# Performance work log

Measured on AMD Instinct MI355X. Metric: run time of the kernel, lower is better.

Reference implementation:

```python
import jax, jax.numpy as jnp
import numpy as np

THRESHOLD = 0.05   # area-ratio cutoff for 'small target'
SMOOTH = 1e-5      # dice smoothing
FG_FRAC = 0.02     # fraction of foreground pixels in synthetic target (< THRESHOLD)


def setup_inputs() -> dict:
    key = jax.random.key(0)
    k1, k2 = jax.random.split(key)
    B, C, H, W = 64, 1, 512, 512
    pred = jax.random.normal(k1, (B, C, H, W), dtype=jnp.float32)
    # sparse binary mask so area_ratio < threshold for (nearly) all samples
    target = (jax.random.uniform(k2, (B, C, H, W)) < FG_FRAC).astype(jnp.float32)
    return {"pred": pred, "target": target}


def reference(pred, target):
    B = pred.shape[0]
    x = pred.reshape(B, -1)    # [B, P] logits
    t = target.reshape(B, -1)  # [B, P] targets in {0,1}

    # per-sample area ratio and validity mask (replaces the Python branch)
    area_ratio = jnp.mean((t > 0.5).astype(jnp.float32), axis=1)  # [B]
    valid = area_ratio < THRESHOLD                                 # [B] bool

    # BCEWithLogits (numerically stable), weighted by clamp(1 + 10*t, max=20)
    bce = jnp.maximum(x, 0.0) - x * t + jnp.log1p(jnp.exp(-jnp.abs(x)))
    pos_weight = jnp.minimum(1.0 + 10.0 * t, 20.0)
    weighted_bce = jnp.mean(bce * pos_weight, axis=1)  # [B]

    # per-sample dice loss
    p = jax.nn.sigmoid(x)
    intersection = jnp.sum(p * t, axis=1)              # [B]
    union = jnp.sum(p, axis=1) + jnp.sum(t, axis=1)    # [B]
    dice_loss = 1.0 - (2.0 * intersection + SMOOTH) / (union + SMOOTH)

    sample_loss = 0.6 * weighted_bce + 0.4 * dice_loss  # [B]

    n_valid = jnp.sum(valid.astype(jnp.float32))
    total = jnp.sum(jnp.where(valid, sample_loss, 0.0))
    return jnp.where(n_valid > 0, total / jnp.maximum(n_valid, 1.0), 0.0)
```

## Files before the change

kernel.cpp:

```cpp
#include <hip/hip_runtime.h>


#define B_SAMPLES 64
#define P_ELEMS   262144
#define P4        (P_ELEMS / 4)
#define BPS       32
#define NBLK      (B_SAMPLES * BPS)
#define TPB       256
#define CHUNK4    (P4 / BPS)
#define ITERS     (CHUNK4 / TPB)
#define BATCH     4

#define LOG2E 1.44269504088896340736f
#define LN2   0.69314718055994530942f

__global__ __launch_bounds__(TPB) void stal_partial(
        const float* __restrict__ pred,
        const float* __restrict__ target,
        float* __restrict__ ws) {
    const int blk    = blockIdx.x;
    const int sample = blk >> 5;
    const int bin    = blk & (BPS - 1);
    const int tid    = threadIdx.x;

    const float4* p4 = reinterpret_cast<const float4*>(pred)
                       + (size_t)sample * P4 + (size_t)bin * CHUNK4;
    const float4* t4 = reinterpret_cast<const float4*>(target)
                       + (size_t)sample * P4 + (size_t)bin * CHUNK4;

    float s_l2w = 0.f, s_xt = 0.f, s_p = 0.f, s_pt = 0.f, s_t = 0.f;

    #pragma unroll
    for (int g = 0; g < ITERS / BATCH; ++g) {
        float4 xv[BATCH], tv[BATCH];
        #pragma unroll
        for (int i = 0; i < BATCH; ++i) {
            xv[i] = p4[tid + (g * BATCH + i) * TPB];
            tv[i] = t4[tid + (g * BATCH + i) * TPB];
        }
        #pragma unroll
        for (int i = 0; i < BATCH; ++i) {
            #pragma unroll
            for (int j = 0; j < 4; ++j) {
                float x = (&xv[i].x)[j];
                float t = (&tv[i].x)[j];
                float u  = __builtin_amdgcn_exp2f(x * LOG2E);
                float a  = 1.f + u;
                float r  = __builtin_amdgcn_rcpf(a);
                float p  = u * r;
                float l2 = __log2f(a);
                float w  = fmaf(10.f, t, 1.f);
                s_l2w = fmaf(l2, w, s_l2w);
                s_xt  = fmaf(x,  t, s_xt);
                s_p  += p;
                s_pt  = fmaf(p, t, s_pt);
                s_t  += t;
            }
        }
    }

    float s_bce = fmaf(LN2, s_l2w, -11.f * s_xt);

    for (int off = 32; off > 0; off >>= 1) {
        s_bce += __shfl_down(s_bce, off);
        s_pt  += __shfl_down(s_pt,  off);
        s_p   += __shfl_down(s_p,   off);
        s_t   += __shfl_down(s_t,   off);
    }

    __shared__ float red[4][4];
    const int wave = tid >> 6;
    const int lane = tid & 63;
    if (lane == 0) {
        red[wave][0] = s_bce; red[wave][1] = s_pt;
        red[wave][2] = s_p;   red[wave][3] = s_t;
    }
    __syncthreads();
    if (tid == 0) {
        float a = 0.f, b = 0.f, c = 0.f, d = 0.f;
        for (int w = 0; w < 4; ++w) {
            a += red[w][0]; b += red[w][1]; c += red[w][2]; d += red[w][3];
        }
        float* o = ws + (size_t)blk * 4;
        o[0] = a; o[1] = b; o[2] = c; o[3] = d;
    }
}

__global__ __launch_bounds__(64) void stal_finalize(
        const float* __restrict__ ws,
        float* __restrict__ out) {
    const int b = threadIdx.x;

    float S0 = 0.f, S1 = 0.f, S2 = 0.f, S3 = 0.f;
    const float4* w4 = reinterpret_cast<const float4*>(ws) + (size_t)b * BPS;
    for (int k = 0; k < BPS; ++k) {
        float4 o = w4[k];
        S0 += o.x; S1 += o.y; S2 += o.z; S3 += o.w;
    }

    const float invP = 1.f / (float)P_ELEMS;
    float area  = S3 * invP;
    bool  valid = area < 0.05f;
    float wbce  = S0 * invP;
    float dice  = 1.f - (2.f * S1 + 1e-5f) / (S2 + S3 + 1e-5f);
    float loss  = 0.6f * wbce + 0.4f * dice;

    float v       = valid ? 1.f : 0.f;
    float contrib = valid ? loss : 0.f;
    for (int off = 32; off > 0; off >>= 1) {
        contrib += __shfl_down(contrib, off);
        v       += __shfl_down(v, off);
    }
    if (b == 0) {
        out[0] = (v > 0.f) ? contrib / fmaxf(v, 1.f) : 0.f;
    }
}

extern "C" void kernel_launch(void* const* d_in, const int* in_sizes, int n_in,
                              void* d_out, int out_size, void* d_ws, size_t ws_size,
                              hipStream_t stream) {
    const float* pred   = (const float*)d_in[0];
    const float* target = (const float*)d_in[1];
    float* out = (float*)d_out;
    float* ws  = (float*)d_ws;

    stal_partial <<<NBLK, TPB, 0, stream>>>(pred, target, ws);
    stal_finalize<<<1, 64, 0, stream>>>(ws, out);
}
```

Measured before the change: 27.90 us.

## Fuse finalize into partial kernel via atomics and last-block counter

Replaces the two-kernel reduction with a single kernel. Each block atomically adds its partial sums into per-sample accumulators, padded to 32 floats apart, then bumps a global counter, and the last block to finish computes the final loss. A hipMemsetAsync zeroes the accumulators and counter before launch, which replaces the second kernel launch with a memset. It also adds a launch_bounds occupancy hint, and the float atomic adds make the summation order nondeterministic.

```diff
diff --git a/kernel.cpp b/kernel.cpp
--- a/kernel.cpp
+++ b/kernel.cpp
@@ -10,14 +10,17 @@
 #define CHUNK4    (P4 / BPS)
 #define ITERS     (CHUNK4 / TPB)
 #define BATCH     4
+#define ACC_STRIDE 32
 
 #define LOG2E 1.44269504088896340736f
 #define LN2   0.69314718055994530942f
 
-__global__ __launch_bounds__(TPB) void stal_partial(
+__global__ __launch_bounds__(TPB, 4) void stal_fused(
         const float* __restrict__ pred,
         const float* __restrict__ target,
-        float* __restrict__ ws) {
+        float* __restrict__ acc,
+        unsigned int* __restrict__ counter,
+        float* __restrict__ out) {
     const int blk    = blockIdx.x;
     const int sample = blk >> 5;
     const int bin    = blk & (BPS - 1);
@@ -69,6 +72,7 @@
     }
 
     __shared__ float red[4][4];
+    __shared__ int   is_last;
     const int wave = tid >> 6;
     const int lane = tid & 63;
     if (lane == 0) {
@@ -81,38 +85,40 @@
         for (int w = 0; w < 4; ++w) {
             a += red[w][0]; b += red[w][1]; c += red[w][2]; d += red[w][3];
         }
-        float* o = ws + (size_t)blk * 4;
-        o[0] = a; o[1] = b; o[2] = c; o[3] = d;
+        float* s = acc + (size_t)sample * ACC_STRIDE;
+        atomicAdd(s + 0, a);
+        atomicAdd(s + 1, b);
+        atomicAdd(s + 2, c);
+        atomicAdd(s + 3, d);
+        asm volatile("s_waitcnt vmcnt(0)" ::: "memory");
+        is_last = (atomicAdd(counter, 1u) == NBLK - 1) ? 1 : 0;
     }
-}
+    __syncthreads();
+    if (!is_last) return;
 
-__global__ __launch_bounds__(64) void stal_finalize(
-        const float* __restrict__ ws,
-        float* __restrict__ out) {
-    const int b = threadIdx.x;
+    if (tid < B_SAMPLES) {
+        float* s = acc + (size_t)tid * ACC_STRIDE;
+        float S0 = atomicAdd(s + 0, 0.f);
+        float S1 = atomicAdd(s + 1, 0.f);
+        float S2 = atomicAdd(s + 2, 0.f);
+        float S3 = atomicAdd(s + 3, 0.f);
 
-    float S0 = 0.f, S1 = 0.f, S2 = 0.f, S3 = 0.f;
-    const float4* w4 = reinterpret_cast<const float4*>(ws) + (size_t)b * BPS;
-    for (int k = 0; k < BPS; ++k) {
-        float4 o = w4[k];
-        S0 += o.x; S1 += o.y; S2 += o.z; S3 += o.w;
-    }
+        const float invP = 1.f / (float)P_ELEMS;
+        float area  = S3 * invP;
+        bool  valid = area < 0.05f;
+        float wbce  = S0 * invP;
+        float dice  = 1.f - (2.f * S1 + 1e-5f) / (S2 + S3 + 1e-5f);
+        float loss  = 0.6f * wbce + 0.4f * dice;
 
-    const float invP = 1.f / (float)P_ELEMS;
-    float area  = S3 * invP;
-    bool  valid = area < 0.05f;
-    float wbce  = S0 * invP;
-    float dice  = 1.f - (2.f * S1 + 1e-5f) / (S2 + S3 + 1e-5f);
-    float loss  = 0.6f * wbce + 0.4f * dice;
-
-    float v       = valid ? 1.f : 0.f;
-    float contrib = valid ? loss : 0.f;
-    for (int off = 32; off > 0; off >>= 1) {
-        contrib += __shfl_down(contrib, off);
-        v       += __shfl_down(v, off);
-    }
-    if (b == 0) {
-        out[0] = (v > 0.f) ? contrib / fmaxf(v, 1.f) : 0.f;
+        float v       = valid ? 1.f : 0.f;
+        float contrib = valid ? loss : 0.f;
+        for (int off = 32; off > 0; off >>= 1) {
+            contrib += __shfl_down(contrib, off);
+            v       += __shfl_down(v, off);
+        }
+        if (tid == 0) {
+            out[0] = (v > 0.f) ? contrib / fmaxf(v, 1.f) : 0.f;
+        }
     }
 }
 
@@ -122,8 +128,11 @@
     const float* pred   = (const float*)d_in[0];
     const float* target = (const float*)d_in[1];
     float* out = (float*)d_out;
-    float* ws  = (float*)d_ws;
+    float* acc = (float*)d_ws;
+    unsigned int* counter = (unsigned int*)((char*)d_ws
+                              + B_SAMPLES * ACC_STRIDE * sizeof(float));
 
-    stal_partial <<<NBLK, TPB, 0, stream>>>(pred, target, ws);
-    stal_finalize<<<1, 64, 0, stream>>>(ws, out);
+    (void)hipMemsetAsync(d_ws, 0, B_SAMPLES * ACC_STRIDE * sizeof(float)
+                                   + sizeof(unsigned int), stream);
+    stal_fused<<<NBLK, TPB, 0, stream>>>(pred, target, acc, counter, out);
 }
```

After: 47.39 us. +69.9%, slower.
